# Kernel optimization log

Measured on AMD Instinct MI355X. Metric: run time of the kernel, lower is better.

## Reference

```python
import jax, jax.numpy as jnp
import numpy as np

B, T, C, Q, NW, MD = 4, 2048, 512, 300, 32, 256
WS, NC, S = 16, 4, 16
L = T - WS + 1  # unfold output length, stride 1, no pad


def _pe(x):
    # standard sinusoidal positional encoding added to x [B,t,d]
    t, d = x.shape[1], x.shape[2]
    pos = jnp.arange(t, dtype=jnp.float32)[:, None]
    div = jnp.exp(jnp.arange(0, d, 2, dtype=jnp.float32) * (-np.log(10000.0) / d))
    ang = pos * div                                   # [t, d//2]
    pe = jnp.stack([jnp.sin(ang), jnp.cos(ang)], axis=-1).reshape(t, d)
    return x + pe[None]


def _mlp(x, w1, b1, w2, b2):
    return jax.nn.relu(x @ w1 + b1) @ w2 + b2


def setup_inputs():
    key = jax.random.key(0)
    ks = iter(jax.random.split(key, 32))

    def lin(k, fin, fout):
        kw, kb = jax.random.split(k)
        return (jax.random.normal(kw, (fin, fout), jnp.float32) / np.sqrt(fin),
                jax.random.normal(kb, (fout,), jnp.float32) * 0.01)

    inp = {}
    inp["vis_feats"] = jax.random.normal(next(ks), (B, T, C), jnp.float32)
    inp["query_feats"] = jax.random.normal(next(ks), (B, NW, Q), jnp.float32)
    inp["vW1"], inp["vb1"] = lin(next(ks), C, C)
    inp["vW2"], inp["vb2"] = lin(next(ks), C, C)
    inp["s1W1"], inp["s1b1"] = lin(next(ks), Q, Q)
    inp["s1W2"], inp["s1b2"] = lin(next(ks), Q, C)
    inp["s2W1"], inp["s2b1"] = lin(next(ks), Q, Q)
    inp["s2W2"], inp["s2b2"] = lin(next(ks), Q, C)
    inp["pW1"], inp["pb1"] = lin(next(ks), NC * C, C)
    inp["pW2"], inp["pb2"] = lin(next(ks), C, 2)
    inp["mW"], inp["mb"] = lin(next(ks), C, MD)
    inp["stW"], inp["stb"] = lin(next(ks), MD * S, S)
    inp["enW"], inp["enb"] = lin(next(ks), MD * S, S)
    inp["vis_len"] = jax.random.randint(next(ks), (B,), L // 2, L + 1, dtype=jnp.int32)
    return inp


def reference(vis_feats, query_feats, vW1, vb1, vW2, vb2,
              s1W1, s1b1, s1W2, s1b2, s2W1, s2b1, s2W2, s2b2,
              pW1, pb1, pW2, pb2, mW, mb, stW, stb, enW, enb, vis_len):
    v = _mlp(_pe(vis_feats), vW1, vb1, vW2, vb2)                # [B,T,C]
    q = _pe(query_feats)
    enc1 = _mlp(q, s1W1, s1b1, s1W2, s1b2)                      # [B,NW,C]
    enc2 = _mlp(q, s2W1, s2b1, s2W2, s2b2)                      # [B,NW,C]
    sim = jnp.einsum('btc,bwc->btw', v, enc1)                   # [B,T,NW]

    widx = jnp.arange(L)[:, None] + jnp.arange(WS)[None, :]     # [L,WS] sliding windows
    vu = v[:, widx, :].reshape(B, L, NC, WS // NC, C).mean(axis=3)       # [B,L,NC,C] avg-pool per chunk
    bel = sim[:, widx, :].reshape(B, L, NC, WS // NC, NW).sum(axis=3)    # [B,L,NC,NW]
    labels = jnp.argmax(bel, axis=3)                            # [B,L,NC] selected word per chunk
    sel = jax.vmap(lambda e, lab: e[lab])(enc2, labels)         # [B,L,NC,C] gather word embeddings
    mod = sel * vu                                              # modulate

    pred = _mlp(mod.reshape(B, L, NC * C), pW1, pb1, pW2, pb2).transpose(0, 2, 1)  # [B,2,L]

    x = (mod @ mW + mb).reshape(B, L * NC, MD)                  # [B,N,MD]
    n = (vis_len * NC).astype(jnp.int32)                        # ragged valid length per batch
    i = jnp.arange(S, dtype=jnp.int32)
    starts = (n[:, None] * i[None, :]) // S                     # adaptive-maxpool bin bounds
    ends = (n[:, None] * (i[None, :] + 1) + S - 1) // S
    j = jnp.arange(L * NC, dtype=jnp.int32)
    cols = []
    for b in range(S):  # S is a small fixed constant (not a data dim)
        m = (j[None, :] >= starts[:, b:b + 1]) & (j[None, :] < ends[:, b:b + 1])  # [B,N]
        cols.append(jnp.max(jnp.where(m[:, :, None], x, -jnp.inf), axis=1))       # [B,MD]
    feat = jnp.stack(cols, axis=2).reshape(B, MD * S)           # [B,MD,S] flattened channel-major
    start = (feat @ stW + stb)[:, :, None]                      # [B,S,1]
    end = (feat @ enW + enb)[:, :, None]                        # [B,S,1]
    return pred, start, end
```

## Files before the change

kernel.cpp:

```cpp
#include <hip/hip_runtime.h>
#include <hip/hip_bf16.h>
#include <math.h>

#define BB 4
#define TT 2048
#define CC 512
#define QQ 300
#define NWW 32
#define MDD 256
#define WSS 16
#define NCC 4
#define SS 16
#define LL (TT - WSS + 1)
#define NSUB 8
#define PUL (TT - 3)

typedef __attribute__((ext_vector_type(8))) short short8;
typedef __attribute__((ext_vector_type(4))) short short4v;
typedef __attribute__((ext_vector_type(4))) float f32x4;

__device__ __forceinline__ void pe_add4(f32x4& v, int t, int gk0)
{
    #pragma unroll
    for (int j = 0; j < 4; j++) {
        int gk = gk0 + j;
        float di = expf((float)(gk & ~1) * (-9.210340371976184f / (float)CC));
        float ang = (float)t * di;
        v[j] += (gk & 1) ? cosf(ang) : sinf(ang);
    }
}

template<int PE>
__global__ __launch_bounds__(256, 2) void gemm_f32_fast(
    const float* __restrict__ A, const float* __restrict__ Bm,
    const float* __restrict__ bias, float* __restrict__ Cm,
    int M, int N, int K, int do_relu)
{
    __shared__ float As[2][32][68];
    __shared__ float Bs[2][32][128];
    const int bm = blockIdx.x * 64;
    const int bn = blockIdx.y * 128;
    const int tid = threadIdx.x;
    const int tx = tid & 31;
    const int ty = tid >> 5;

    float acc[8][4] = {};
    f32x4 pa[2], pb[4];
    int am[2], akq[2], bkr[4], bnq[4];
    #pragma unroll
    for (int i = 0; i < 2; i++) {
        int idx = i * 256 + tid;
        am[i] = idx >> 3; akq[i] = (idx & 7) * 4;
    }
    #pragma unroll
    for (int i = 0; i < 4; i++) {
        int idx = i * 256 + tid;
        bkr[i] = idx >> 5; bnq[i] = (idx & 31) * 4;
    }

    const int nk0 = K / 32;
    #pragma unroll
    for (int i = 0; i < 2; i++) {
        pa[i] = *(const f32x4*)(A + (size_t)(bm + am[i]) * K + akq[i]);
        if (PE) pe_add4(pa[i], (bm + am[i]) & (TT - 1), akq[i]);
    }
    #pragma unroll
    for (int i = 0; i < 4; i++)
        pb[i] = *(const f32x4*)(Bm + (size_t)bkr[i] * N + bn + bnq[i]);

    int buf = 0;
    for (int k0i = 0; ; k0i++) {
        #pragma unroll
        for (int i = 0; i < 2; i++)
            #pragma unroll
            for (int j = 0; j < 4; j++) As[buf][akq[i] + j][am[i]] = pa[i][j];
        #pragma unroll
        for (int i = 0; i < 4; i++)
            *(f32x4*)&Bs[buf][bkr[i]][bnq[i]] = pb[i];
        __syncthreads();
        if (k0i + 1 < nk0) {
            int k0 = (k0i + 1) * 32;
            #pragma unroll
            for (int i = 0; i < 2; i++) {
                pa[i] = *(const f32x4*)(A + (size_t)(bm + am[i]) * K + k0 + akq[i]);
                if (PE) pe_add4(pa[i], (bm + am[i]) & (TT - 1), k0 + akq[i]);
            }
            #pragma unroll
            for (int i = 0; i < 4; i++)
                pb[i] = *(const f32x4*)(Bm + (size_t)(k0 + bkr[i]) * N + bn + bnq[i]);
        }
        #pragma unroll 8
        for (int kk = 0; kk < 32; kk++) {
            f32x4 a0 = *(const f32x4*)&As[buf][kk][ty * 8];
            f32x4 a1 = *(const f32x4*)&As[buf][kk][ty * 8 + 4];
            f32x4 b0 = *(const f32x4*)&Bs[buf][kk][tx * 4];
            #pragma unroll
            for (int i2 = 0; i2 < 4; i2++)
                #pragma unroll
                for (int j2 = 0; j2 < 4; j2++) {
                    acc[i2][j2]     += a0[i2] * b0[j2];
                    acc[i2 + 4][j2] += a1[i2] * b0[j2];
                }
        }
        buf ^= 1;
        if (k0i + 1 == nk0) break;
    }

    #pragma unroll
    for (int i = 0; i < 8; i++) {
        int gm = bm + ty * 8 + i;
        f32x4 o;
        #pragma unroll
        for (int j = 0; j < 4; j++) {
            float v0 = acc[i][j] + bias[bn + tx * 4 + j];
            if (do_relu) v0 = fmaxf(v0, 0.f);
            o[j] = v0;
        }
        *(f32x4*)(Cm + (size_t)gm * N + bn + tx * 4) = o;
    }
}

__global__ __launch_bounds__(64) void sgemm_dual(
    const float* __restrict__ A,
    const float* __restrict__ W1, const float* __restrict__ b1, float* __restrict__ C1,
    const float* __restrict__ W2, const float* __restrict__ b2, float* __restrict__ C2,
    int M, int N, int K, int do_relu)
{
    int id = blockIdx.x * 64 + threadIdx.x;
    if (id >= M * N) return;
    const float* B = blockIdx.y ? W2 : W1;
    const float* bias = blockIdx.y ? b2 : b1;
    float* C = blockIdx.y ? C2 : C1;
    int m = id / N, n = id % N;
    const float* a = A + (size_t)m * K;
    const float* b = B + n;
    float acc = 0.f;
    int k = 0;
    for (; k + 10 <= K; k += 10) {
        float av[10], bv[10];
        #pragma unroll
        for (int u = 0; u < 10; u++) av[u] = a[k + u];
        #pragma unroll
        for (int u = 0; u < 10; u++) bv[u] = b[(size_t)(k + u) * N];
        #pragma unroll
        for (int u = 0; u < 10; u++) acc = fmaf(av[u], bv[u], acc);
    }
    for (; k < K; k++) acc = fmaf(a[k], b[(size_t)k * N], acc);
    float val = acc + bias[n];
    if (do_relu) val = fmaxf(val, 0.f);
    C[id] = val;
}

__global__ __launch_bounds__(256) void gemm_bf16_kernel(
    const short* __restrict__ A,
    const short* __restrict__ Bt,
    const float* __restrict__ bias, float* __restrict__ C,
    int M, int N, int K, int do_relu)
{
    __shared__ short As[128][40];
    __shared__ short Bs[128][40];
    const int bm = blockIdx.x * 128;
    const int bn = blockIdx.y * 128;
    const int tid = threadIdx.x;
    const int wave = tid >> 6, lane = tid & 63;
    const int wm = (wave & 1) * 64, wn = (wave >> 1) * 64;
    const int l15 = lane & 15, lk = (lane >> 4) * 8;
    const int srow = tid >> 2;
    const int scol = (tid & 3) * 8;

    f32x4 acc[4][4] = {};

    for (int k0 = 0; k0 < K; k0 += 32) {
        #pragma unroll
        for (int p = 0; p < 2; p++) {
            int row = p * 64 + srow;
            short8 av = {};
            int gm = bm + row;
            if (gm < M) av = *(const short8*)(A + (size_t)gm * K + k0 + scol);
            *(short8*)&As[row][scol] = av;
            short8 bv = {};
            int gn = bn + row;
            if (gn < N) bv = *(const short8*)(Bt + (size_t)gn * K + k0 + scol);
            *(short8*)&Bs[row][scol] = bv;
        }
        __syncthreads();

        short8 af[4], bf[4];
        #pragma unroll
        for (int mi = 0; mi < 4; mi++)
            af[mi] = *(const short8*)&As[wm + mi * 16 + l15][lk];
        #pragma unroll
        for (int ni = 0; ni < 4; ni++)
            bf[ni] = *(const short8*)&Bs[wn + ni * 16 + l15][lk];
        #pragma unroll
        for (int mi = 0; mi < 4; mi++)
            #pragma unroll
            for (int ni = 0; ni < 4; ni++)
                acc[mi][ni] = __builtin_amdgcn_mfma_f32_16x16x32_bf16(
                    af[mi], bf[ni], acc[mi][ni], 0, 0, 0);
        __syncthreads();
    }

    #pragma unroll
    for (int mi = 0; mi < 4; mi++) {
        int row0 = bm + wm + mi * 16 + (lane >> 4) * 4;
        #pragma unroll
        for (int ni = 0; ni < 4; ni++) {
            int col = bn + wn + ni * 16 + l15;
            float bsv = bias ? bias[col] : 0.f;
            #pragma unroll
            for (int r = 0; r < 4; r++) {
                int grow = row0 + r;
                if (grow >= M) continue;
                float val = acc[mi][ni][r] + bsv;
                if (do_relu) val = fmaxf(val, 0.f);
                C[(size_t)grow * N + col] = val;
            }
        }
    }
}

__global__ __launch_bounds__(256) void convT2_kernel(
    const float* __restrict__ src, __hip_bfloat16* __restrict__ dst,
    int K, int N)
{
    __shared__ float t[32][33];
    int c = threadIdx.x & 31, r4 = threadIdx.x >> 5;
    int n0 = blockIdx.x * 32, k0 = blockIdx.y * 32;
    #pragma unroll
    for (int rr = 0; rr < 32; rr += 8)
        t[rr + r4][c] = src[(size_t)(k0 + rr + r4) * N + n0 + c];
    __syncthreads();
    #pragma unroll
    for (int rr = 0; rr < 32; rr += 8)
        dst[(size_t)(n0 + rr + r4) * K + k0 + c] = __float2bfloat16(t[c][rr + r4]);
}

__global__ void qpe_kernel(const float* __restrict__ q, float* __restrict__ out)
{
    int idx = blockIdx.x * 256 + threadIdx.x;
    if (idx >= BB * NWW * QQ) return;
    int qi = idx % QQ;
    int w  = (idx / QQ) % NWW;
    float di = expf((float)(qi & ~1) * (-9.210340371976184f / (float)QQ));
    float ang = (float)w * di;
    out[idx] = q[idx] + ((qi & 1) ? cosf(ang) : sinf(ang));
}

__global__ __launch_bounds__(256) void sim_kernel(
    const float* __restrict__ v, const float* __restrict__ enc1,
    float* __restrict__ sim)
{
    __shared__ float vs[8][CC];
    int blk = blockIdx.x;
    int b  = blk / (TT / 8);
    int t0 = (blk % (TT / 8)) * 8;
    int tid = threadIdx.x;
    for (int i = tid; i < 8 * (CC / 4); i += 256) {
        int r = i / (CC / 4), c = i % (CC / 4);
        *(f32x4*)&vs[r][c * 4] =
            *(const f32x4*)(v + ((size_t)b * TT + t0 + r) * CC + c * 4);
    }
    __syncthreads();
    int w  = tid & 31;
    int tt = tid >> 5;
    const f32x4* e4 = (const f32x4*)(enc1 + ((size_t)b * NWW + w) * CC);
    const f32x4* v4 = (const f32x4*)vs[tt];
    float s = 0.f;
    #pragma unroll 4
    for (int kq = 0; kq < CC / 4; kq++) {
        f32x4 vv = v4[kq], ee = e4[kq];
        s = fmaf(vv[0], ee[0], s);
        s = fmaf(vv[1], ee[1], s);
        s = fmaf(vv[2], ee[2], s);
        s = fmaf(vv[3], ee[3], s);
    }
    sim[((size_t)b * TT + t0 + tt) * NWW + w] = s;
}

__global__ __launch_bounds__(256) void pu_kernel(
    const float* __restrict__ v, float* __restrict__ pu)
{
    int idx = blockIdx.x * 256 + threadIdx.x;
    if (idx >= BB * PUL * (CC / 4)) return;
    int q = idx % (CC / 4);
    int t = (idx / (CC / 4)) % PUL;
    int b = idx / ((CC / 4) * PUL);
    const float* vp = v + ((size_t)b * TT + t) * CC + q * 4;
    f32x4 r0 = *(const f32x4*)vp;
    f32x4 r1 = *(const f32x4*)(vp + CC);
    f32x4 r2 = *(const f32x4*)(vp + 2 * CC);
    f32x4 r3 = *(const f32x4*)(vp + 3 * CC);
    f32x4 o;
    #pragma unroll
    for (int j = 0; j < 4; j++)
        o[j] = 0.25f * (((r0[j] + r1[j]) + r2[j]) + r3[j]);
    *(f32x4*)(pu + ((size_t)b * PUL + t) * CC + q * 4) = o;
}

__global__ __launch_bounds__(256) void mod_kernel(
    const float* __restrict__ pu, const float* __restrict__ sim,
    const float* __restrict__ enc2, __hip_bfloat16* __restrict__ modb)
{
    int blk = blockIdx.x;
    int b = blk / LL, l = blk % LL;
    int tid = threadIdx.x;
    int cch = tid >> 6;
    int lane = tid & 63;
    int t0 = l + cch * 4;

    int w = lane & 31;
    const float* sp = sim + ((size_t)b * TT + t0) * NWW + w;
    float bel = sp[0] + sp[NWW] + sp[2 * NWW] + sp[3 * NWW];
    int idx = w;
    #pragma unroll
    for (int m = 1; m < 32; m <<= 1) {
        float ov = __shfl_xor(bel, m);
        int   oi = __shfl_xor(idx, m);
        if (ov > bel || (ov == bel && oi < idx)) { bel = ov; idx = oi; }
    }

    const f32x4* e2 = (const f32x4*)(enc2 + ((size_t)b * NWW + idx) * CC);
    const f32x4* pq = (const f32x4*)(pu + ((size_t)b * PUL + t0) * CC);
    __hip_bfloat16* mp = modb + (((size_t)blk) * NCC + cch) * CC;
    #pragma unroll
    for (int q = lane; q < CC / 4; q += 64) {
        f32x4 e = e2[q], p = pq[q];
        short4v o;
        #pragma unroll
        for (int j = 0; j < 4; j++) {
            __hip_bfloat16 h = __float2bfloat16(e[j] * p[j]);
            o[j] = *(short*)&h;
        }
        *(short4v*)(mp + q * 4) = o;
    }
}

__global__ __launch_bounds__(256) void pred2w_kernel(
    const float* __restrict__ hpred, const float* __restrict__ pW2,
    const float* __restrict__ pb2, float* __restrict__ out)
{
    int row = blockIdx.x * 4 + (threadIdx.x >> 6);
    if (row >= BB * LL) return;
    int lane = threadIdx.x & 63;
    const float* h = hpred + (size_t)row * CC + lane * 8;
    f32x4 h0 = *(const f32x4*)h;
    f32x4 h1 = *(const f32x4*)(h + 4);
    const float* wp = pW2 + lane * 16;
    f32x4 w0 = *(const f32x4*)wp;
    f32x4 w1 = *(const f32x4*)(wp + 4);
    f32x4 w2 = *(const f32x4*)(wp + 8);
    f32x4 w3 = *(const f32x4*)(wp + 12);
    float s0 = h0[0]*w0[0] + h0[1]*w0[2] + h0[2]*w1[0] + h0[3]*w1[2]
             + h1[0]*w2[0] + h1[1]*w2[2] + h1[2]*w3[0] + h1[3]*w3[2];
    float s1 = h0[0]*w0[1] + h0[1]*w0[3] + h0[2]*w1[1] + h0[3]*w1[3]
             + h1[0]*w2[1] + h1[1]*w2[3] + h1[2]*w3[1] + h1[3]*w3[3];
    #pragma unroll
    for (int m = 32; m; m >>= 1) {
        s0 += __shfl_xor(s0, m);
        s1 += __shfl_xor(s1, m);
    }
    if (lane == 0) {
        int b = row / LL, l = row % LL;
        out[((size_t)b * 2 + 0) * LL + l] = s0 + pb2[0];
        out[((size_t)b * 2 + 1) * LL + l] = s1 + pb2[1];
    }
}

__global__ __launch_bounds__(256) void pool1_kernel(
    const float* __restrict__ x, const int* __restrict__ vis_len,
    float* __restrict__ scratch)
{
    int blk = blockIdx.x;
    int sub = blk % NSUB;
    int s   = (blk / NSUB) % SS;
    int b   = blk / (NSUB * SS);
    int n = vis_len[b] * NCC;
    int st = (n * s) / SS;
    int en = (n * (s + 1) + SS - 1) / SS;
    int len = en - st;
    int j0 = st + (len * sub) / NSUB;
    int j1 = st + (len * (sub + 1)) / NSUB;
    int md = threadIdx.x;
    float m = -INFINITY;
    const float* xp = x + (size_t)b * (LL * NCC) * MDD + md;
    for (int j = j0; j < j1; j++) m = fmaxf(m, xp[(size_t)j * MDD]);
    scratch[(size_t)blk * MDD + md] = m;
}

__global__ __launch_bounds__(256) void pool2_kernel(
    const float* __restrict__ scratch, float* __restrict__ feat)
{
    int blk = blockIdx.x;
    int md = threadIdx.x;
    const float* sp = scratch + (size_t)blk * NSUB * MDD + md;
    float m = sp[0];
    #pragma unroll
    for (int i = 1; i < NSUB; i++) m = fmaxf(m, sp[(size_t)i * MDD]);
    int b = blk / SS, s = blk % SS;
    feat[(size_t)b * MDD * SS + md * SS + s] = m;
}

__global__ void stend_kernel(const float* __restrict__ feat,
                             const float* __restrict__ stW, const float* __restrict__ stb,
                             const float* __restrict__ enW, const float* __restrict__ enb,
                             float* __restrict__ out)
{
    int bid = blockIdx.x;
    int which = bid >> 6;
    int r = bid & 63;
    int b = r >> 4, s = r & 15;
    int lane = threadIdx.x;
    const float* W  = which ? enW : stW;
    const float* bb = which ? enb : stb;
    const float* f  = feat + (size_t)b * MDD * SS;
    float acc = 0.f;
    for (int k = lane; k < MDD * SS; k += 64) acc += f[k] * W[(size_t)k * SS + s];
    #pragma unroll
    for (int m = 32; m; m >>= 1) acc += __shfl_xor(acc, m);
    if (lane == 0)
        out[(size_t)BB * 2 * LL + which * (BB * SS) + b * SS + s] = acc + bb[s];
}

extern "C" void kernel_launch(void* const* d_in, const int* in_sizes, int n_in,
                              void* d_out, int out_size, void* d_ws, size_t ws_size,
                              hipStream_t stream)
{
    const float* vis  = (const float*)d_in[0];
    const float* qf   = (const float*)d_in[1];
    const float* vW1  = (const float*)d_in[2];  const float* vb1 = (const float*)d_in[3];
    const float* vW2  = (const float*)d_in[4];  const float* vb2 = (const float*)d_in[5];
    const float* s1W1 = (const float*)d_in[6];  const float* s1b1= (const float*)d_in[7];
    const float* s1W2 = (const float*)d_in[8];  const float* s1b2= (const float*)d_in[9];
    const float* s2W1 = (const float*)d_in[10]; const float* s2b1= (const float*)d_in[11];
    const float* s2W2 = (const float*)d_in[12]; const float* s2b2= (const float*)d_in[13];
    const float* pW1  = (const float*)d_in[14]; const float* pb1 = (const float*)d_in[15];
    const float* pW2  = (const float*)d_in[16]; const float* pb2 = (const float*)d_in[17];
    const float* mW   = (const float*)d_in[18]; const float* mb  = (const float*)d_in[19];
    const float* stW  = (const float*)d_in[20]; const float* stb = (const float*)d_in[21];
    const float* enW  = (const float*)d_in[22]; const float* enb = (const float*)d_in[23];
    const int*   vlen = (const int*)d_in[24];
    float* out = (float*)d_out;

    float* ws   = (float*)d_ws;
    float* h1   = ws;
    float* v    = h1   + (size_t)BB * TT * CC;
    float* qpe  = v    + (size_t)BB * TT * CC;
    float* qh   = qpe  + (size_t)BB * NWW * QQ;
    float* enc1 = qh   + (size_t)BB * NWW * QQ;
    float* enc2 = enc1 + (size_t)BB * NWW * CC;
    float* sim  = enc2 + (size_t)BB * NWW * CC;
    float* feat = sim  + (size_t)BB * TT * NWW;
    float* x    = feat + (size_t)BB * MDD * SS;
    float* fend = x    + (size_t)BB * LL * NCC * MDD;
    __hip_bfloat16* modb = (__hip_bfloat16*)fend;
    __hip_bfloat16* pW1t = modb + (size_t)BB * LL * NCC * CC;
    __hip_bfloat16* mWt  = pW1t + (size_t)CC * (NCC * CC);

    const int MT = BB * TT;
    const int ML = BB * LL;
    const int MX = BB * LL * NCC;

    convT2_kernel<<<dim3(CC / 32, (NCC * CC) / 32), 256, 0, stream>>>(pW1, pW1t, NCC * CC, CC);
    convT2_kernel<<<dim3(MDD / 32, CC / 32), 256, 0, stream>>>(mW, mWt, CC, MDD);

    gemm_f32_fast<1><<<dim3(MT / 64, CC / 128), 256, 0, stream>>>(
        vis, vW1, vb1, h1, MT, CC, CC, 1);
    gemm_f32_fast<0><<<dim3(MT / 64, CC / 128), 256, 0, stream>>>(
        h1, vW2, vb2, v, MT, CC, CC, 0);
    qpe_kernel<<<(BB * NWW * QQ + 255) / 256, 256, 0, stream>>>(qf, qpe);
    sgemm_dual<<<dim3((BB * NWW * QQ + 63) / 64, 2), 64, 0, stream>>>(
        qpe, s1W1, s1b1, qh, s2W1, s2b1, qh + (size_t)BB * NWW * QQ, 0, 0, 0, 1);

    ;
    float* qh2 = enc2 + (size_t)BB * NWW * CC;
    qh2 = (float*)(mWt + (size_t)CC * MDD);
    sgemm_dual<<<dim3((BB * NWW * QQ + 63) / 64, 2), 64, 0, stream>>>(
        qpe, s1W1, s1b1, qh, s2W1, s2b1, qh2, BB * NWW, QQ, QQ, 1);
    sgemm_dual<<<dim3((BB * NWW * CC + 63) / 64, 2), 64, 0, stream>>>(
        qh, s1W2, s1b2, enc1, s1W2, s1b2, enc1, BB * NWW, CC, QQ, 0);
    sgemm_dual<<<dim3((BB * NWW * CC + 63) / 64, 1), 64, 0, stream>>>(
        qh2, s2W2, s2b2, enc2, s2W2, s2b2, enc2, BB * NWW, CC, QQ, 0);
    sim_kernel<<<BB * (TT / 8), 256, 0, stream>>>(v, enc1, sim);
    pu_kernel<<<(BB * PUL * (CC / 4) + 255) / 256, 256, 0, stream>>>(v, h1);
    mod_kernel<<<BB * LL, 256, 0, stream>>>(h1, sim, enc2, modb);
    gemm_bf16_kernel<<<dim3((MX + 127) / 128, MDD / 128), 256, 0, stream>>>(
        (const short*)modb, (const short*)mWt, mb, x, MX, MDD, CC, 0);
    gemm_bf16_kernel<<<dim3((ML + 127) / 128, CC / 128), 256, 0, stream>>>(
        (const short*)modb, (const short*)pW1t, pb1, h1, ML, CC, NCC * CC, 1);
    pred2w_kernel<<<(ML + 3) / 4, 256, 0, stream>>>(h1, pW2, pb2, out);
    pool1_kernel<<<BB * SS * NSUB, 256, 0, stream>>>(x, vlen, sim);
    pool2_kernel<<<BB * SS, 256, 0, stream>>>(sim, feat);
    stend_kernel<<<128, 64, 0, stream>>>(feat, stW, stb, enW, enb, out);
}
```

Before: 424.5 us.

## Enlarge f32 GEMM tile to 128x128 and fuse query MLP branch into one kernel

The fp32 vision-MLP GEMM moves from 64x128 to 128x128 block tiles, with each thread computing an 8x8 micro-tile instead of 8x4. This raises arithmetic intensity per shared-memory load but doubles accumulator registers and lowers the occupancy hint to one block per SM. Separately, the query positional-encoding add and both two-layer query MLPs are fused into a single per-row kernel that keeps intermediates in shared memory. This replaces four launches, including a redundant no-op launch, and drops the global round trips for the intermediates, at the cost of only 128 blocks doing serial dot products.

```diff
diff --git a/kernel.cpp b/kernel.cpp
--- a/kernel.cpp
+++ b/kernel.cpp
@@ -31,75 +31,69 @@
 }
 
 template<int PE>
-__global__ __launch_bounds__(256, 2) void gemm_f32_fast(
+__global__ __launch_bounds__(256, 1) void gemm_f32_fast(
     const float* __restrict__ A, const float* __restrict__ Bm,
     const float* __restrict__ bias, float* __restrict__ Cm,
     int M, int N, int K, int do_relu)
 {
-    __shared__ float As[2][32][68];
-    __shared__ float Bs[2][32][128];
-    const int bm = blockIdx.x * 64;
+    __shared__ float As[2][32][132];
+    __shared__ float Bs[2][32][132];
+    const int bm = blockIdx.x * 128;
     const int bn = blockIdx.y * 128;
     const int tid = threadIdx.x;
-    const int tx = tid & 31;
-    const int ty = tid >> 5;
-
-    float acc[8][4] = {};
-    f32x4 pa[2], pb[4];
-    int am[2], akq[2], bkr[4], bnq[4];
-    #pragma unroll
-    for (int i = 0; i < 2; i++) {
-        int idx = i * 256 + tid;
-        am[i] = idx >> 3; akq[i] = (idx & 7) * 4;
-    }
+    const int tx = tid & 15;
+    const int ty = tid >> 4;
+
+    float acc[8][8] = {};
+    f32x4 pa[4], pb[4];
+    int am[4], akq[4], bkr[4], bnq[4];
     #pragma unroll
     for (int i = 0; i < 4; i++) {
         int idx = i * 256 + tid;
-        bkr[i] = idx >> 5; bnq[i] = (idx & 31) * 4;
+        am[i]  = idx >> 3;  akq[i] = (idx & 7) * 4;
+        bkr[i] = idx >> 5;  bnq[i] = (idx & 31) * 4;
     }
 
     const int nk0 = K / 32;
     #pragma unroll
-    for (int i = 0; i < 2; i++) {
+    for (int i = 0; i < 4; i++) {
         pa[i] = *(const f32x4*)(A + (size_t)(bm + am[i]) * K + akq[i]);
         if (PE) pe_add4(pa[i], (bm + am[i]) & (TT - 1), akq[i]);
-    }
-    #pragma unroll
-    for (int i = 0; i < 4; i++)
         pb[i] = *(const f32x4*)(Bm + (size_t)bkr[i] * N + bn + bnq[i]);
+    }
 
     int buf = 0;
     for (int k0i = 0; ; k0i++) {
         #pragma unroll
-        for (int i = 0; i < 2; i++)
+        for (int i = 0; i < 4; i++) {
             #pragma unroll
             for (int j = 0; j < 4; j++) As[buf][akq[i] + j][am[i]] = pa[i][j];
-        #pragma unroll
-        for (int i = 0; i < 4; i++)
             *(f32x4*)&Bs[buf][bkr[i]][bnq[i]] = pb[i];
+        }
         __syncthreads();
         if (k0i + 1 < nk0) {
             int k0 = (k0i + 1) * 32;
             #pragma unroll
-            for (int i = 0; i < 2; i++) {
+            for (int i = 0; i < 4; i++) {
                 pa[i] = *(const f32x4*)(A + (size_t)(bm + am[i]) * K + k0 + akq[i]);
                 if (PE) pe_add4(pa[i], (bm + am[i]) & (TT - 1), k0 + akq[i]);
+                pb[i] = *(const f32x4*)(Bm + (size_t)(k0 + bkr[i]) * N + bn + bnq[i]);
             }
-            #pragma unroll
-            for (int i = 0; i < 4; i++)
-                pb[i] = *(const f32x4*)(Bm + (size_t)(k0 + bkr[i]) * N + bn + bnq[i]);
-        }
-        #pragma unroll 8
+        }
+        #pragma unroll 4
         for (int kk = 0; kk < 32; kk++) {
             f32x4 a0 = *(const f32x4*)&As[buf][kk][ty * 8];
             f32x4 a1 = *(const f32x4*)&As[buf][kk][ty * 8 + 4];
             f32x4 b0 = *(const f32x4*)&Bs[buf][kk][tx * 4];
+            f32x4 b1 = *(const f32x4*)&Bs[buf][kk][64 + tx * 4];
             #pragma unroll
             for (int i2 = 0; i2 < 4; i2++)
                 #pragma unroll
                 for (int j2 = 0; j2 < 4; j2++) {
-                    acc[i2][j2]     += a0[i2] * b0[j2];
-                    acc[i2 + 4][j2] += a1[i2] * b0[j2];
+                    acc[i2][j2]         += a0[i2] * b0[j2];
+                    acc[i2][j2 + 4]     += a0[i2] * b1[j2];
+                    acc[i2 + 4][j2]     += a1[i2] * b0[j2];
+                    acc[i2 + 4][j2 + 4] += a1[i2] * b1[j2];
                 }
         }
         buf ^= 1;
@@ -109,46 +103,95 @@
     #pragma unroll
     for (int i = 0; i < 8; i++) {
         int gm = bm + ty * 8 + i;
-        f32x4 o;
+        f32x4 o0, o1;
         #pragma unroll
         for (int j = 0; j < 4; j++) {
-            float v0 = acc[i][j] + bias[bn + tx * 4 + j];
-            if (do_relu) v0 = fmaxf(v0, 0.f);
-            o[j] = v0;
-        }
-        *(f32x4*)(Cm + (size_t)gm * N + bn + tx * 4) = o;
-    }
-}
-
-__global__ __launch_bounds__(64) void sgemm_dual(
-    const float* __restrict__ A,
-    const float* __restrict__ W1, const float* __restrict__ b1, float* __restrict__ C1,
-    const float* __restrict__ W2, const float* __restrict__ b2, float* __restrict__ C2,
-    int M, int N, int K, int do_relu)
-{
-    int id = blockIdx.x * 64 + threadIdx.x;
-    if (id >= M * N) return;
-    const float* B = blockIdx.y ? W2 : W1;
-    const float* bias = blockIdx.y ? b2 : b1;
-    float* C = blockIdx.y ? C2 : C1;
-    int m = id / N, n = id % N;
-    const float* a = A + (size_t)m * K;
-    const float* b = B + n;
-    float acc = 0.f;
-    int k = 0;
-    for (; k + 10 <= K; k += 10) {
-        float av[10], bv[10];
-        #pragma unroll
-        for (int u = 0; u < 10; u++) av[u] = a[k + u];
-        #pragma unroll
-        for (int u = 0; u < 10; u++) bv[u] = b[(size_t)(k + u) * N];
-        #pragma unroll
-        for (int u = 0; u < 10; u++) acc = fmaf(av[u], bv[u], acc);
-    }
-    for (; k < K; k++) acc = fmaf(a[k], b[(size_t)k * N], acc);
-    float val = acc + bias[n];
-    if (do_relu) val = fmaxf(val, 0.f);
-    C[id] = val;
+            float v0 = acc[i][j]     + bias[bn + tx * 4 + j];
+            float v1 = acc[i][j + 4] + bias[bn + 64 + tx * 4 + j];
+            if (do_relu) { v0 = fmaxf(v0, 0.f); v1 = fmaxf(v1, 0.f); }
+            o0[j] = v0; o1[j] = v1;
+        }
+        *(f32x4*)(Cm + (size_t)gm * N + bn + tx * 4)      = o0;
+        *(f32x4*)(Cm + (size_t)gm * N + bn + 64 + tx * 4) = o1;
+    }
+}
+
+__global__ __launch_bounds__(256) void query_fused(
+    const float* __restrict__ qf,
+    const float* __restrict__ s1W1, const float* __restrict__ s1b1,
+    const float* __restrict__ s1W2, const float* __restrict__ s1b2,
+    const float* __restrict__ s2W1, const float* __restrict__ s2b1,
+    const float* __restrict__ s2W2, const float* __restrict__ s2b2,
+    float* __restrict__ enc1, float* __restrict__ enc2)
+{
+    __shared__ float qrow[QQ];
+    __shared__ float h1row[QQ];
+    __shared__ float h2row[QQ];
+    const int m = blockIdx.x;
+    const int w = m % NWW;
+    const int tid = threadIdx.x;
+
+    for (int qi = tid; qi < QQ; qi += 256) {
+        float di = expf((float)(qi & ~1) * (-9.210340371976184f / (float)QQ));
+        float ang = (float)w * di;
+        qrow[qi] = qf[(size_t)m * QQ + qi] + ((qi & 1) ? cosf(ang) : sinf(ang));
+    }
+    __syncthreads();
+
+    for (int n = tid; n < QQ; n += 256) {
+        const float* b1p = s1W1 + n;
+        const float* b2p = s2W1 + n;
+        float a1 = 0.f, a2 = 0.f;
+        int k = 0;
+        for (; k + 10 <= QQ; k += 10) {
+            float av[10], bv1[10], bv2[10];
+            #pragma unroll
+            for (int u = 0; u < 10; u++) av[u] = qrow[k + u];
+            #pragma unroll
+            for (int u = 0; u < 10; u++) bv1[u] = b1p[(size_t)(k + u) * QQ];
+            #pragma unroll
+            for (int u = 0; u < 10; u++) bv2[u] = b2p[(size_t)(k + u) * QQ];
+            #pragma unroll
+            for (int u = 0; u < 10; u++) a1 = fmaf(av[u], bv1[u], a1);
+            #pragma unroll
+            for (int u = 0; u < 10; u++) a2 = fmaf(av[u], bv2[u], a2);
+        }
+        for (; k < QQ; k++) {
+            a1 = fmaf(qrow[k], b1p[(size_t)k * QQ], a1);
+            a2 = fmaf(qrow[k], b2p[(size_t)k * QQ], a2);
+        }
+        h1row[n] = fmaxf(a1 + s1b1[n], 0.f);
+        h2row[n] = fmaxf(a2 + s2b1[n], 0.f);
+    }
+    __syncthreads();
+
+    for (int n = tid; n < CC; n += 256) {
+        const float* b1p = s1W2 + n;
+        const float* b2p = s2W2 + n;
+        float a1 = 0.f, a2 = 0.f;
+        int k = 0;
+        for (; k + 10 <= QQ; k += 10) {
+            float av1[10], av2[10], bv1[10], bv2[10];
+            #pragma unroll
+            for (int u = 0; u < 10; u++) av1[u] = h1row[k + u];
+            #pragma unroll
+            for (int u = 0; u < 10; u++) av2[u] = h2row[k + u];
+            #pragma unroll
+            for (int u = 0; u < 10; u++) bv1[u] = b1p[(size_t)(k + u) * CC];
+            #pragma unroll
+            for (int u = 0; u < 10; u++) bv2[u] = b2p[(size_t)(k + u) * CC];
+            #pragma unroll
+            for (int u = 0; u < 10; u++) a1 = fmaf(av1[u], bv1[u], a1);
+            #pragma unroll
+            for (int u = 0; u < 10; u++) a2 = fmaf(av2[u], bv2[u], a2);
+        }
+        for (; k < QQ; k++) {
+            a1 = fmaf(h1row[k], b1p[(size_t)k * CC], a1);
+            a2 = fmaf(h2row[k], b2p[(size_t)k * CC], a2);
+        }
+        enc1[(size_t)m * CC + n] = a1 + s1b2[n];
+        enc2[(size_t)m * CC + n] = a2 + s2b2[n];
+    }
 }
 
 __global__ __launch_bounds__(256) void gemm_bf16_kernel(
@@ -234,17 +277,6 @@
     #pragma unroll
     for (int rr = 0; rr < 32; rr += 8)
         dst[(size_t)(n0 + rr + r4) * K + k0 + c] = __float2bfloat16(t[c][rr + r4]);
-}
-
-__global__ void qpe_kernel(const float* __restrict__ q, float* __restrict__ out)
-{
-    int idx = blockIdx.x * 256 + threadIdx.x;
-    if (idx >= BB * NWW * QQ) return;
-    int qi = idx % QQ;
-    int w  = (idx / QQ) % NWW;
-    float di = expf((float)(qi & ~1) * (-9.210340371976184f / (float)QQ));
-    float ang = (float)w * di;
-    out[idx] = q[idx] + ((qi & 1) ? cosf(ang) : sinf(ang));
 }
 
 __global__ __launch_bounds__(256) void sim_kernel(
@@ -464,23 +496,12 @@
     convT2_kernel<<<dim3(CC / 32, (NCC * CC) / 32), 256, 0, stream>>>(pW1, pW1t, NCC * CC, CC);
     convT2_kernel<<<dim3(MDD / 32, CC / 32), 256, 0, stream>>>(mW, mWt, CC, MDD);
 
-    gemm_f32_fast<1><<<dim3(MT / 64, CC / 128), 256, 0, stream>>>(
+    gemm_f32_fast<1><<<dim3(MT / 128, CC / 128), 256, 0, stream>>>(
         vis, vW1, vb1, h1, MT, CC, CC, 1);
-    gemm_f32_fast<0><<<dim3(MT / 64, CC / 128), 256, 0, stream>>>(
+    gemm_f32_fast<0><<<dim3(MT / 128, CC / 128), 256, 0, stream>>>(
         h1, vW2, vb2, v, MT, CC, CC, 0);
-    qpe_kernel<<<(BB * NWW * QQ + 255) / 256, 256, 0, stream>>>(qf, qpe);
-    sgemm_dual<<<dim3((BB * NWW * QQ + 63) / 64, 2), 64, 0, stream>>>(
-        qpe, s1W1, s1b1, qh, s2W1, s2b1, qh + (size_t)BB * NWW * QQ, 0, 0, 0, 1);
-
-    ;
-    float* qh2 = enc2 + (size_t)BB * NWW * CC;
-    qh2 = (float*)(mWt + (size_t)CC * MDD);
-    sgemm_dual<<<dim3((BB * NWW * QQ + 63) / 64, 2), 64, 0, stream>>>(
-        qpe, s1W1, s1b1, qh, s2W1, s2b1, qh2, BB * NWW, QQ, QQ, 1);
-    sgemm_dual<<<dim3((BB * NWW * CC + 63) / 64, 2), 64, 0, stream>>>(
-        qh, s1W2, s1b2, enc1, s1W2, s1b2, enc1, BB * NWW, CC, QQ, 0);
-    sgemm_dual<<<dim3((BB * NWW * CC + 63) / 64, 1), 64, 0, stream>>>(
-        qh2, s2W2, s2b2, enc2, s2W2, s2b2, enc2, BB * NWW, CC, QQ, 0);
+    query_fused<<<BB * NWW, 256, 0, stream>>>(
+        qf, s1W1, s1b1, s1W2, s1b2, s2W1, s2b1, s2W2, s2b2, enc1, enc2);
     sim_kernel<<<BB * (TT / 8), 256, 0, stream>>>(v, enc1, sim);
     pu_kernel<<<(BB * PUL * (CC / 4) + 255) / 256, 256, 0, stream>>>(v, h1);
     mod_kernel<<<BB * LL, 256, 0, stream>>>(h1, sim, enc2, modb);
```

After: 464.7 us. 9.5% more time.

## Enlarge fp32 GEMM tiles to 128x128 and merge query MLP launches

Applied to the files above, without the earlier changes.

The fp32 visual MLP GEMM now uses 128x128 output tiles, so each thread computes an 8x8 accumulator instead of 8x4. This raises arithmetic intensity per shared-memory load, at the cost of more registers and lower occupancy (launch bounds now allow one block). The query-side MLP is also consolidated: a no-op launch is removed, and the second layers of both branches run in one dual launch that takes separate A inputs. This cuts the number of kernel launches.

```diff
diff --git a/kernel.cpp b/kernel.cpp
--- a/kernel.cpp
+++ b/kernel.cpp
@@ -31,75 +31,69 @@
 }
 
 template<int PE>
-__global__ __launch_bounds__(256, 2) void gemm_f32_fast(
+__global__ __launch_bounds__(256, 1) void gemm_f32_fast(
     const float* __restrict__ A, const float* __restrict__ Bm,
     const float* __restrict__ bias, float* __restrict__ Cm,
     int M, int N, int K, int do_relu)
 {
-    __shared__ float As[2][32][68];
-    __shared__ float Bs[2][32][128];
-    const int bm = blockIdx.x * 64;
+    __shared__ float As[2][32][132];
+    __shared__ float Bs[2][32][132];
+    const int bm = blockIdx.x * 128;
     const int bn = blockIdx.y * 128;
     const int tid = threadIdx.x;
-    const int tx = tid & 31;
-    const int ty = tid >> 5;
-
-    float acc[8][4] = {};
-    f32x4 pa[2], pb[4];
-    int am[2], akq[2], bkr[4], bnq[4];
-    #pragma unroll
-    for (int i = 0; i < 2; i++) {
-        int idx = i * 256 + tid;
-        am[i] = idx >> 3; akq[i] = (idx & 7) * 4;
-    }
+    const int tx = tid & 15;
+    const int ty = tid >> 4;
+
+    float acc[8][8] = {};
+    f32x4 pa[4], pb[4];
+    int am[4], akq[4], bkr[4], bnq[4];
     #pragma unroll
     for (int i = 0; i < 4; i++) {
         int idx = i * 256 + tid;
-        bkr[i] = idx >> 5; bnq[i] = (idx & 31) * 4;
+        am[i]  = idx >> 3;  akq[i] = (idx & 7) * 4;
+        bkr[i] = idx >> 5;  bnq[i] = (idx & 31) * 4;
     }
 
     const int nk0 = K / 32;
     #pragma unroll
-    for (int i = 0; i < 2; i++) {
+    for (int i = 0; i < 4; i++) {
         pa[i] = *(const f32x4*)(A + (size_t)(bm + am[i]) * K + akq[i]);
         if (PE) pe_add4(pa[i], (bm + am[i]) & (TT - 1), akq[i]);
-    }
-    #pragma unroll
-    for (int i = 0; i < 4; i++)
         pb[i] = *(const f32x4*)(Bm + (size_t)bkr[i] * N + bn + bnq[i]);
+    }
 
     int buf = 0;
     for (int k0i = 0; ; k0i++) {
         #pragma unroll
-        for (int i = 0; i < 2; i++)
+        for (int i = 0; i < 4; i++) {
             #pragma unroll
             for (int j = 0; j < 4; j++) As[buf][akq[i] + j][am[i]] = pa[i][j];
-        #pragma unroll
-        for (int i = 0; i < 4; i++)
             *(f32x4*)&Bs[buf][bkr[i]][bnq[i]] = pb[i];
+        }
         __syncthreads();
         if (k0i + 1 < nk0) {
             int k0 = (k0i + 1) * 32;
             #pragma unroll
-            for (int i = 0; i < 2; i++) {
+            for (int i = 0; i < 4; i++) {
                 pa[i] = *(const f32x4*)(A + (size_t)(bm + am[i]) * K + k0 + akq[i]);
                 if (PE) pe_add4(pa[i], (bm + am[i]) & (TT - 1), k0 + akq[i]);
+                pb[i] = *(const f32x4*)(Bm + (size_t)(k0 + bkr[i]) * N + bn + bnq[i]);
             }
-            #pragma unroll
-            for (int i = 0; i < 4; i++)
-                pb[i] = *(const f32x4*)(Bm + (size_t)(k0 + bkr[i]) * N + bn + bnq[i]);
-        }
-        #pragma unroll 8
+        }
+        #pragma unroll 4
         for (int kk = 0; kk < 32; kk++) {
             f32x4 a0 = *(const f32x4*)&As[buf][kk][ty * 8];
             f32x4 a1 = *(const f32x4*)&As[buf][kk][ty * 8 + 4];
             f32x4 b0 = *(const f32x4*)&Bs[buf][kk][tx * 4];
+            f32x4 b1 = *(const f32x4*)&Bs[buf][kk][64 + tx * 4];
             #pragma unroll
             for (int i2 = 0; i2 < 4; i2++)
                 #pragma unroll
                 for (int j2 = 0; j2 < 4; j2++) {
-                    acc[i2][j2]     += a0[i2] * b0[j2];
-                    acc[i2 + 4][j2] += a1[i2] * b0[j2];
+                    acc[i2][j2]         += a0[i2] * b0[j2];
+                    acc[i2][j2 + 4]     += a0[i2] * b1[j2];
+                    acc[i2 + 4][j2]     += a1[i2] * b0[j2];
+                    acc[i2 + 4][j2 + 4] += a1[i2] * b1[j2];
                 }
         }
         buf ^= 1;
@@ -109,25 +103,40 @@
     #pragma unroll
     for (int i = 0; i < 8; i++) {
         int gm = bm + ty * 8 + i;
-        f32x4 o;
+        f32x4 o0, o1;
         #pragma unroll
         for (int j = 0; j < 4; j++) {
-            float v0 = acc[i][j] + bias[bn + tx * 4 + j];
-            if (do_relu) v0 = fmaxf(v0, 0.f);
-            o[j] = v0;
-        }
-        *(f32x4*)(Cm + (size_t)gm * N + bn + tx * 4) = o;
-    }
-}
-
-__global__ __launch_bounds__(64) void sgemm_dual(
-    const float* __restrict__ A,
-    const float* __restrict__ W1, const float* __restrict__ b1, float* __restrict__ C1,
-    const float* __restrict__ W2, const float* __restrict__ b2, float* __restrict__ C2,
+            float v0 = acc[i][j]     + bias[bn + tx * 4 + j];
+            float v1 = acc[i][j + 4] + bias[bn + 64 + tx * 4 + j];
+            if (do_relu) { v0 = fmaxf(v0, 0.f); v1 = fmaxf(v1, 0.f); }
+            o0[j] = v0; o1[j] = v1;
+        }
+        *(f32x4*)(Cm + (size_t)gm * N + bn + tx * 4)      = o0;
+        *(f32x4*)(Cm + (size_t)gm * N + bn + 64 + tx * 4) = o1;
+    }
+}
+
+__global__ void qpe_kernel(const float* __restrict__ q, float* __restrict__ out)
+{
+    int idx = blockIdx.x * 256 + threadIdx.x;
+    if (idx >= BB * NWW * QQ) return;
+    int qi = idx % QQ;
+    int w  = (idx / QQ) % NWW;
+    float di = expf((float)(qi & ~1) * (-9.210340371976184f / (float)QQ));
+    float ang = (float)w * di;
+    out[idx] = q[idx] + ((qi & 1) ? cosf(ang) : sinf(ang));
+}
+
+__global__ __launch_bounds__(64) void sgemm_dual2(
+    const float* __restrict__ A1, const float* __restrict__ W1,
+    const float* __restrict__ b1, float* __restrict__ C1,
+    const float* __restrict__ A2, const float* __restrict__ W2,
+    const float* __restrict__ b2, float* __restrict__ C2,
     int M, int N, int K, int do_relu)
 {
     int id = blockIdx.x * 64 + threadIdx.x;
     if (id >= M * N) return;
+    const float* A = blockIdx.y ? A2 : A1;
     const float* B = blockIdx.y ? W2 : W1;
     const float* bias = blockIdx.y ? b2 : b1;
     float* C = blockIdx.y ? C2 : C1;
@@ -234,17 +243,6 @@
     #pragma unroll
     for (int rr = 0; rr < 32; rr += 8)
         dst[(size_t)(n0 + rr + r4) * K + k0 + c] = __float2bfloat16(t[c][rr + r4]);
-}
-
-__global__ void qpe_kernel(const float* __restrict__ q, float* __restrict__ out)
-{
-    int idx = blockIdx.x * 256 + threadIdx.x;
-    if (idx >= BB * NWW * QQ) return;
-    int qi = idx % QQ;
-    int w  = (idx / QQ) % NWW;
-    float di = expf((float)(qi & ~1) * (-9.210340371976184f / (float)QQ));
-    float ang = (float)w * di;
-    out[idx] = q[idx] + ((qi & 1) ? cosf(ang) : sinf(ang));
 }
 
 __global__ __launch_bounds__(256) void sim_kernel(
@@ -456,6 +454,7 @@
     __hip_bfloat16* modb = (__hip_bfloat16*)fend;
     __hip_bfloat16* pW1t = modb + (size_t)BB * LL * NCC * CC;
     __hip_bfloat16* mWt  = pW1t + (size_t)CC * (NCC * CC);
+    float* qh2 = (float*)(mWt + (size_t)CC * MDD);
 
     const int MT = BB * TT;
     const int ML = BB * LL;
@@ -464,23 +463,15 @@
     convT2_kernel<<<dim3(CC / 32, (NCC * CC) / 32), 256, 0, stream>>>(pW1, pW1t, NCC * CC, CC);
     convT2_kernel<<<dim3(MDD / 32, CC / 32), 256, 0, stream>>>(mW, mWt, CC, MDD);
 
-    gemm_f32_fast<1><<<dim3(MT / 64, CC / 128), 256, 0, stream>>>(
+    gemm_f32_fast<1><<<dim3(MT / 128, CC / 128), 256, 0, stream>>>(
         vis, vW1, vb1, h1, MT, CC, CC, 1);
-    gemm_f32_fast<0><<<dim3(MT / 64, CC / 128), 256, 0, stream>>>(
+    gemm_f32_fast<0><<<dim3(MT / 128, CC / 128), 256, 0, stream>>>(
         h1, vW2, vb2, v, MT, CC, CC, 0);
     qpe_kernel<<<(BB * NWW * QQ + 255) / 256, 256, 0, stream>>>(qf, qpe);
-    sgemm_dual<<<dim3((BB * NWW * QQ + 63) / 64, 2), 64, 0, stream>>>(
-        qpe, s1W1, s1b1, qh, s2W1, s2b1, qh + (size_t)BB * NWW * QQ, 0, 0, 0, 1);
-
-    ;
-    float* qh2 = enc2 + (size_t)BB * NWW * CC;
-    qh2 = (float*)(mWt + (size_t)CC * MDD);
-    sgemm_dual<<<dim3((BB * NWW * QQ + 63) / 64, 2), 64, 0, stream>>>(
-        qpe, s1W1, s1b1, qh, s2W1, s2b1, qh2, BB * NWW, QQ, QQ, 1);
-    sgemm_dual<<<dim3((BB * NWW * CC + 63) / 64, 2), 64, 0, stream>>>(
-        qh, s1W2, s1b2, enc1, s1W2, s1b2, enc1, BB * NWW, CC, QQ, 0);
-    sgemm_dual<<<dim3((BB * NWW * CC + 63) / 64, 1), 64, 0, stream>>>(
-        qh2, s2W2, s2b2, enc2, s2W2, s2b2, enc2, BB * NWW, CC, QQ, 0);
+    sgemm_dual2<<<dim3((BB * NWW * QQ + 63) / 64, 2), 64, 0, stream>>>(
+        qpe, s1W1, s1b1, qh, qpe, s2W1, s2b1, qh2, BB * NWW, QQ, QQ, 1);
+    sgemm_dual2<<<dim3((BB * NWW * CC + 63) / 64, 2), 64, 0, stream>>>(
+        qh, s1W2, s1b2, enc1, qh2, s2W2, s2b2, enc2, BB * NWW, CC, QQ, 0);
     sim_kernel<<<BB * (TT / 8), 256, 0, stream>>>(v, enc1, sim);
     pu_kernel<<<(BB * PUL * (CC / 4) + 255) / 256, 256, 0, stream>>>(v, h1);
     mod_kernel<<<BB * LL, 256, 0, stream>>>(h1, sim, enc2, modb);
```

Result: faster. 411.5 us (-3.1%).
